# Performance work log

Hardware: AMD Instinct MI355X
Metric: run time of the kernel (lower is better)

Reference implementation:

```python
import jax, jax.numpy as jnp
import numpy as np

EMB_DIM = 4096
INNER = 1024
VOCAB = 32000
NPRED = 3
B, N = 2, 512
EPS = 1e-6
# weighting constants from MLPSpeculator.__init__
STATE_W = 0.5 ** (0.5 / NPRED)
ALPHA = float(np.sqrt((1.0 - STATE_W ** 2) * (INNER / 2.0)) / STATE_W)  # emb_weight / state_weight


def _ln(x, w, b):
    # LayerNormParameterized with use_mean=False (fms default): RMS-style norm + scale + shift
    x = x * jax.lax.rsqrt(jnp.mean(x * x, axis=-1, keepdims=True) + EPS)
    return x * w + b


def setup_inputs() -> dict:
    key = jax.random.key(0)
    ks = jax.random.split(key, 8)
    s = 1.0 / np.sqrt(INNER)  # reset_parameters init scale
    return {
        "state": jax.random.normal(ks[0], (B, N, EMB_DIM), jnp.float32),
        "inds": jax.random.randint(ks[1], (B, N + NPRED), 0, VOCAB, dtype=jnp.int32),
        "emb_w": jax.random.normal(ks[2], (NPRED, VOCAB, INNER), jnp.float32) * s,
        "proj0_w": jax.random.normal(ks[3], (INNER, EMB_DIM), jnp.float32) * s,
        "proj_w": jax.random.normal(ks[4], (NPRED - 1, INNER, INNER), jnp.float32) * s,
        "head_w": jax.random.normal(ks[5], (NPRED, VOCAB, INNER), jnp.float32) * s,
        "ln_w": jnp.ones((NPRED, INNER), jnp.float32),
        "ln_b": jnp.zeros((NPRED, INNER), jnp.float32),
    }


def reference(state, inds, emb_w, proj0_w, proj_w, head_w, ln_w, ln_b):
    n = state.shape[1]
    outs = []
    for i in range(NPRED):
        z = emb_w[i][inds[:, i:i + n]]                      # [b, n, inner] gather
        W = proj0_w if i == 0 else proj_w[i - 1]            # [inner, emb_dim] or [inner, inner]
        state = jnp.einsum('bnd,id->bni', state, W)
        state = state + ALPHA * z                           # torch.add(..., alpha=emb_w/state_w)
        state = jax.nn.gelu(_ln(state, ln_w[i], ln_b[i]), approximate=False)
        outs.append(jnp.einsum('bni,vi->bnv', state, head_w[i]))  # logits [b, n, vocab]
    return jnp.stack(outs, axis=0)                          # [n_predict, b, n, vocab]
```

## Files before the change

kernel.cpp:

```cpp
#include <hip/hip_runtime.h>
#include <hip/hip_bf16.h>
#include <math.h>

#define EMB_DIM 4096
#define INNER   1024
#define VOCAB   32000
#define NPRED   3
#define SEQ     512
#define TOKENS  1024

typedef __attribute__((ext_vector_type(8))) short bf16x8;
typedef __attribute__((ext_vector_type(4))) float f32x4;

__device__ inline void gload_lds16(const void* g, void* l) {
  __builtin_amdgcn_global_load_lds(
      (const __attribute__((address_space(1))) void*)g,
      (__attribute__((address_space(3))) void*)l, 16, 0, 0);
}

__device__ inline unsigned short f2bf(float f) {
  unsigned u = __float_as_uint(f);
  u += 0x7fffu + ((u >> 16) & 1u);
  return (unsigned short)(u >> 16);
}

__global__ void cvt_kernel(const float4* __restrict__ in, ushort4* __restrict__ out, int n4) {
  int stride = gridDim.x * blockDim.x;
  for (int i = blockIdx.x * blockDim.x + threadIdx.x; i < n4; i += stride) {
    float4 v = in[i];
    ushort4 o;
    o.x = f2bf(v.x); o.y = f2bf(v.y); o.z = f2bf(v.z); o.w = f2bf(v.w);
    out[i] = o;
  }
}

__global__ __launch_bounds__(256) void proj_cvt(const __hip_bfloat16* __restrict__ A,
                                                const __hip_bfloat16* __restrict__ Bw,
                                                float* __restrict__ C, int K,
                                                const float4* __restrict__ cvsrc,
                                                ushort4* __restrict__ cvdst, int n4) {
  if (blockIdx.x >= 64) {
    for (int i = (blockIdx.x - 64) * 256 + threadIdx.x; i < n4; i += 960 * 256) {
      float4 v = cvsrc[i];
      ushort4 o;
      o.x = f2bf(v.x); o.y = f2bf(v.y); o.z = f2bf(v.z); o.w = f2bf(v.w);
      cvdst[i] = o;
    }
    return;
  }
  __shared__ char smem[16384];
  char* As = smem;
  char* Bs = smem + 8192;

  const int tid  = threadIdx.x;
  const int lane = tid & 63;
  const int wave = tid >> 6;
  const int wm = wave >> 1, wn = wave & 1;

  const int bm = (blockIdx.x >> 3) * 128;
  const int bn = (blockIdx.x & 7) * 128;
  const int N = 1024;

  const char* Ag = (const char*)(A  + (size_t)(bm + (tid >> 2)) * K + (tid & 3) * 8);
  const char* Bg = (const char*)(Bw + (size_t)(bn + (tid >> 2)) * K + (tid & 3) * 8);
  const size_t rowskip = (size_t)64 * K * 2;

  f32x4 acc[4][4] = {};

  const int fa = (wm * 64 + (lane & 15)) * 64 + (lane >> 4) * 16;
  const int fb = (wn * 64 + (lane & 15)) * 64 + (lane >> 4) * 16;

  for (int k0 = 0; k0 < K; k0 += 32) {
    gload_lds16(Ag,           As + tid * 16);
    gload_lds16(Ag + rowskip, As + 4096 + tid * 16);
    gload_lds16(Bg,           Bs + tid * 16);
    gload_lds16(Bg + rowskip, Bs + 4096 + tid * 16);
    Ag += 64; Bg += 64;
    __syncthreads();

    bf16x8 af[4], bfv[4];
#pragma unroll
    for (int m = 0; m < 4; ++m) af[m]  = *(const bf16x8*)(As + fa + m * 1024);
#pragma unroll
    for (int n = 0; n < 4; ++n) bfv[n] = *(const bf16x8*)(Bs + fb + n * 1024);
#pragma unroll
    for (int m = 0; m < 4; ++m)
#pragma unroll
      for (int n = 0; n < 4; ++n)
        acc[m][n] = __builtin_amdgcn_mfma_f32_16x16x32_bf16(af[m], bfv[n], acc[m][n], 0, 0, 0);
    __syncthreads();
  }

  const int r0 = bm + wm * 64 + (lane >> 4) * 4;
  const int c0 = bn + wn * 64 + (lane & 15);
#pragma unroll
  for (int m = 0; m < 4; ++m)
#pragma unroll
    for (int n = 0; n < 4; ++n) {
      float* Cp = C + (size_t)(r0 + m * 16) * N + (c0 + n * 16);
#pragma unroll
      for (int r = 0; r < 4; ++r)
        Cp[(size_t)r * N] = acc[m][n][r];
    }
}

__global__ __launch_bounds__(512, 2) void gemm256(const __hip_bfloat16* __restrict__ A,
                                                  const __hip_bfloat16* __restrict__ B,
                                                  float* __restrict__ C,
                                                  int M, int N, int K) {
  __shared__ char smem[65536];
  const int tid  = threadIdx.x;
  const int lane = tid & 63;
  const int wave = tid >> 6;
  const int wm = wave >> 2;
  const int wn = wave & 3;

  const int MT = M >> 8;
  const int nwg = gridDim.x;
  const int o = blockIdx.x;
  const int q = nwg >> 3, r = nwg & 7;
  const int xcd = o & 7, idx = o >> 3;
  const int wg = (xcd < r ? xcd * (q + 1) : r * (q + 1) + (xcd - r) * q) + idx;
  const int bm = (wg % MT) * 256;
  const int bn = (wg / MT) * 256;

  f32x4 acc[8][4] = {};

  const int sl   = (lane >> 4) ^ ((lane >> 1) & 3);
  const int aoff = (wm * 128 + (lane & 15)) * 64 + sl * 16;
  const int boff = (wn * 64  + (lane & 15)) * 64 + sl * 16;

#define STAGE_T(PTR, BASEROW, LDSBASE, KT_)                                     \
  {                                                                             \
    _Pragma("unroll")                                                           \
    for (int c = 0; c < 2; ++c) {                                               \
      int chunk = c * 512 + tid;                                                \
      int row = chunk >> 2;                                                     \
      int s = (chunk & 3) ^ ((row >> 1) & 3);                                   \
      gload_lds16(PTR + (size_t)((BASEROW) + row) * K + (KT_) * 32 + s * 8,     \
                  smem + (LDSBASE) + chunk * 16);                               \
    }                                                                           \
  }

  STAGE_T(A, bm, 0,     0)
  STAGE_T(B, bn, 32768, 0)
  STAGE_T(A, bm, 16384, 1)
  STAGE_T(B, bn, 49152, 1)

  const int KT = K >> 5;
  for (int t = 0; t < KT; ++t) {
    const int b = t & 1;
    const char* Ab = smem + b * 16384;
    const char* Bb = smem + 32768 + b * 16384;

    asm volatile("s_waitcnt vmcnt(4)" ::: "memory");
    __builtin_amdgcn_s_barrier();

    bf16x8 af[8], bfv[4];
#pragma unroll
    for (int m = 0; m < 8; ++m) af[m]  = *(const bf16x8*)(Ab + aoff + m * 1024);
#pragma unroll
    for (int n = 0; n < 4; ++n) bfv[n] = *(const bf16x8*)(Bb + boff + n * 1024);

    asm volatile("s_waitcnt lgkmcnt(0)" ::: "memory");
    __builtin_amdgcn_sched_barrier(0);
    __builtin_amdgcn_s_barrier();

    int pk = (t + 2 < KT) ? t + 2 : KT - 1;
    STAGE_T(A, bm, b * 16384, pk)
    STAGE_T(B, bn, 32768 + b * 16384, pk)

    __builtin_amdgcn_s_setprio(1);
#pragma unroll
    for (int m = 0; m < 8; ++m)
#pragma unroll
      for (int n = 0; n < 4; ++n)
        acc[m][n] = __builtin_amdgcn_mfma_f32_16x16x32_bf16(af[m], bfv[n], acc[m][n], 0, 0, 0);
    __builtin_amdgcn_s_setprio(0);
    __builtin_amdgcn_sched_barrier(0);
  }
  asm volatile("s_waitcnt vmcnt(0)" ::: "memory");

  const int r0 = bm + wm * 128 + (lane >> 4) * 4;
  const int c0 = bn + wn * 64 + (lane & 15);
#pragma unroll
  for (int m = 0; m < 8; ++m)
#pragma unroll
    for (int n = 0; n < 4; ++n) {
      float* Cp = C + (size_t)(r0 + m * 16) * N + (c0 + n * 16);
#pragma unroll
      for (int rr = 0; rr < 4; ++rr)
        Cp[(size_t)rr * N] = acc[m][n][rr];
    }
#undef STAGE_T
}

__global__ __launch_bounds__(256) void fuse_ln_gelu(const float* __restrict__ ns,
    const float* __restrict__ emb,
    const int* __restrict__ inds,
    const float* __restrict__ lnw, const float* __restrict__ lnb,
    ushort4* __restrict__ out_bf16,
    int i, float alpha)
{
  const int t = blockIdx.x;
  const int b = t >> 9, n = t & 511;
  const int idx = inds[b * (SEQ + NPRED) + n + i];

  const float4* x = (const float4*)(ns + (size_t)t * INNER);
  const float4* z = (const float4*)(emb + (size_t)idx * INNER);
  const int j = threadIdx.x;

  float4 xv = x[j], zv = z[j];
  float4 v;
  v.x = xv.x + alpha * zv.x;
  v.y = xv.y + alpha * zv.y;
  v.z = xv.z + alpha * zv.z;
  v.w = xv.w + alpha * zv.w;

  float ss = v.x * v.x + v.y * v.y + v.z * v.z + v.w * v.w;
#pragma unroll
  for (int o = 32; o > 0; o >>= 1) ss += __shfl_down(ss, o);
  __shared__ float red[4];
  if ((threadIdx.x & 63) == 0) red[threadIdx.x >> 6] = ss;
  __syncthreads();
  float total = red[0] + red[1] + red[2] + red[3];
  float r = rsqrtf(total * (1.0f / INNER) + 1e-6f);

  float4 wv = ((const float4*)lnw)[j];
  float4 bv = ((const float4*)lnb)[j];
  const float inv_sqrt2 = 0.70710678118654752f;
  ushort4 o;
  float y;
  y = v.x * r * wv.x + bv.x; o.x = f2bf(0.5f * y * (1.0f + erff(y * inv_sqrt2)));
  y = v.y * r * wv.y + bv.y; o.y = f2bf(0.5f * y * (1.0f + erff(y * inv_sqrt2)));
  y = v.z * r * wv.z + bv.z; o.z = f2bf(0.5f * y * (1.0f + erff(y * inv_sqrt2)));
  y = v.w * r * wv.w + bv.w; o.w = f2bf(0.5f * y * (1.0f + erff(y * inv_sqrt2)));

  out_bf16[(size_t)t * (INNER / 4) + j] = o;
}

extern "C" void kernel_launch(void* const* d_in, const int* in_sizes, int n_in,
                              void* d_out, int out_size, void* d_ws, size_t ws_size,
                              hipStream_t stream) {
  const float* state = (const float*)d_in[0];
  const int*   inds  = (const int*)d_in[1];
  const float* emb_w = (const float*)d_in[2];
  const float* proj0 = (const float*)d_in[3];
  const float* projw = (const float*)d_in[4];
  const float* headw = (const float*)d_in[5];
  const float* lnw   = (const float*)d_in[6];
  const float* lnb   = (const float*)d_in[7];
  float* out = (float*)d_out;

  char* ws = (char*)d_ws;
  __hip_bfloat16* stateA = (__hip_bfloat16*)(ws);
  __hip_bfloat16* stateI = (__hip_bfloat16*)(ws + 8388608);
  float*          nsf    = (float*)        (ws + 10485760);
  __hip_bfloat16* p0b    = (__hip_bfloat16*)(ws + 14680064);
  __hip_bfloat16* pwb    = (__hip_bfloat16*)(ws + 23068672);
  __hip_bfloat16* hb     = (__hip_bfloat16*)(ws + 27262976);

  double sw = pow(0.5, 1.0 / 6.0);
  float alpha = (float)(sqrt((1.0 - sw * sw) * (INNER / 2.0)) / sw);

  auto cvt = [&](const float* src, __hip_bfloat16* dst, size_t n) {
    int n4 = (int)(n / 4);
    int blocks = (n4 + 255) / 256;
    if (blocks > 2048) blocks = 2048;
    cvt_kernel<<<dim3(blocks), dim3(256), 0, stream>>>((const float4*)src, (ushort4*)dst, n4);
  };

  cvt(state, stateA, (size_t)TOKENS * EMB_DIM);
  cvt(proj0, p0b, (size_t)INNER * EMB_DIM);
  cvt(projw, pwb, (size_t)2 * INNER * INNER);

  for (int i = 0; i < NPRED; ++i) {
    const __hip_bfloat16* Ab = (i == 0) ? stateA : stateI;
    const __hip_bfloat16* Bb = (i == 0) ? p0b : pwb + (size_t)(i - 1) * INNER * INNER;
    int K = (i == 0) ? EMB_DIM : INNER;

    proj_cvt<<<dim3(1024), dim3(256), 0, stream>>>(Ab, Bb, nsf, K,
        (const float4*)(headw + (size_t)i * VOCAB * INNER), (ushort4*)hb,
        (int)((size_t)VOCAB * INNER / 4));

    fuse_ln_gelu<<<dim3(TOKENS), dim3(256), 0, stream>>>(nsf,
        emb_w + (size_t)i * VOCAB * INNER, inds,
        lnw + i * INNER, lnb + i * INNER, (ushort4*)stateI, i, alpha);

    gemm256<<<dim3(500), dim3(512), 0, stream>>>(stateI, hb,
        out + (size_t)i * TOKENS * VOCAB, TOKENS, VOCAB, INNER);
  }
}
```

Baseline: 452.0 us.

## Deepen gemm256 LDS pipeline to four stages and split MFMA into halves

Result: faster. 439.1 us (-2.9%).

```diff
diff --git a/kernel.cpp b/kernel.cpp
--- a/kernel.cpp
+++ b/kernel.cpp
@@ -108,7 +108,7 @@
                                                   const __hip_bfloat16* __restrict__ B,
                                                   float* __restrict__ C,
                                                   int M, int N, int K) {
-  __shared__ char smem[65536];
+  __shared__ char smem[131072];
   const int tid  = threadIdx.x;
   const int lane = tid & 63;
   const int wave = tid >> 6;
@@ -142,40 +142,53 @@
     }                                                                           \
   }
 
-  STAGE_T(A, bm, 0,     0)
-  STAGE_T(B, bn, 32768, 0)
-  STAGE_T(A, bm, 16384, 1)
-  STAGE_T(B, bn, 49152, 1)
+  STAGE_T(A, bm, 0,             0)
+  STAGE_T(B, bn, 65536,         0)
+  STAGE_T(A, bm, 16384,         1)
+  STAGE_T(B, bn, 65536 + 16384, 1)
+  STAGE_T(A, bm, 32768,         2)
+  STAGE_T(B, bn, 65536 + 32768, 2)
 
   const int KT = K >> 5;
   for (int t = 0; t < KT; ++t) {
-    const int b = t & 1;
-    const char* Ab = smem + b * 16384;
-    const char* Bb = smem + 32768 + b * 16384;
-
-    asm volatile("s_waitcnt vmcnt(4)" ::: "memory");
+    const int bc = (t & 3) * 16384;
+    const int bs = ((t + 3) & 3) * 16384;
+    const char* Ab = smem + bc;
+    const char* Bb = smem + 65536 + bc;
+
+    asm volatile("s_waitcnt vmcnt(8)" ::: "memory");
     __builtin_amdgcn_s_barrier();
 
-    bf16x8 af[8], bfv[4];
-#pragma unroll
-    for (int m = 0; m < 8; ++m) af[m]  = *(const bf16x8*)(Ab + aoff + m * 1024);
+    const int pk = (t + 3 < KT) ? t + 3 : KT - 1;
+
+    bf16x8 af0[4], bfv[4];
+#pragma unroll
+    for (int m = 0; m < 4; ++m) af0[m] = *(const bf16x8*)(Ab + aoff + m * 1024);
 #pragma unroll
     for (int n = 0; n < 4; ++n) bfv[n] = *(const bf16x8*)(Bb + boff + n * 1024);
-
+    STAGE_T(A, bm, bs, pk)
     asm volatile("s_waitcnt lgkmcnt(0)" ::: "memory");
     __builtin_amdgcn_sched_barrier(0);
-    __builtin_amdgcn_s_barrier();
-
-    int pk = (t + 2 < KT) ? t + 2 : KT - 1;
-    STAGE_T(A, bm, b * 16384, pk)
-    STAGE_T(B, bn, 32768 + b * 16384, pk)
-
     __builtin_amdgcn_s_setprio(1);
 #pragma unroll
-    for (int m = 0; m < 8; ++m)
+    for (int m = 0; m < 4; ++m)
 #pragma unroll
       for (int n = 0; n < 4; ++n)
-        acc[m][n] = __builtin_amdgcn_mfma_f32_16x16x32_bf16(af[m], bfv[n], acc[m][n], 0, 0, 0);
+        acc[m][n] = __builtin_amdgcn_mfma_f32_16x16x32_bf16(af0[m], bfv[n], acc[m][n], 0, 0, 0);
+    __builtin_amdgcn_s_setprio(0);
+
+    bf16x8 af1[4];
+#pragma unroll
+    for (int m = 0; m < 4; ++m) af1[m] = *(const bf16x8*)(Ab + aoff + (m + 4) * 1024);
+    STAGE_T(B, bn, 65536 + bs, pk)
+    asm volatile("s_waitcnt lgkmcnt(0)" ::: "memory");
+    __builtin_amdgcn_sched_barrier(0);
+    __builtin_amdgcn_s_setprio(1);
+#pragma unroll
+    for (int m = 0; m < 4; ++m)
+#pragma unroll
+      for (int n = 0; n < 4; ++n)
+        acc[m + 4][n] = __builtin_amdgcn_mfma_f32_16x16x32_bf16(af1[m], bfv[n], acc[m + 4][n], 0, 0, 0);
     __builtin_amdgcn_s_setprio(0);
     __builtin_amdgcn_sched_barrier(0);
   }
```
